# Optimization experiments

Measured on AMD Instinct MI355X. Metric: run time of the kernel, lower is better.

The kernel has to match this reference:

```python
import jax, jax.numpy as jnp
import numpy as np

RADIUS = 51  # odd-ified from 50
WEIGHT = 0.5
THRESHOLD = 10.0


def _gaussian_kernel_2d(k: int) -> np.ndarray:
    # Replicates cv2.getGaussianKernel(k, 0): sigma = 0.3*((k-1)*0.5 - 1) + 0.8
    sigma = 0.3 * ((k - 1) * 0.5 - 1.0) + 0.8
    x = np.arange(k, dtype=np.float64) - (k - 1) / 2.0
    g = np.exp(-(x ** 2) / (2.0 * sigma ** 2))
    g = g / g.sum()
    return np.outer(g, g).astype(np.float32)  # (k, k)


def filter2d(img, kernel):
    # img: (b, c, h, w), kernel: (k, k); depthwise 'same' conv (symmetric zero pad)
    b, c, h, w = img.shape
    k = kernel.shape[-1]
    p = k // 2
    x = img.reshape(b * c, 1, h, w)
    w2 = kernel.reshape(1, 1, k, k).astype(img.dtype)
    out = jax.lax.conv_general_dilated(
        x, w2,
        window_strides=(1, 1),
        padding=[(p, p), (p, p)],
        dimension_numbers=("NCHW", "OIHW", "NCHW"),
    )
    return out.reshape(b, c, h, w)


def setup_inputs() -> dict:
    key = jax.random.key(0)
    img = jax.random.uniform(key, (16, 3, 512, 512), dtype=jnp.float32)
    kernel = jnp.asarray(_gaussian_kernel_2d(RADIUS))
    return {"img": img, "kernel": kernel}


def reference(img, kernel):
    blur = filter2d(img, kernel)
    residual = img - blur
    mask = (jnp.abs(residual) * 255.0 > THRESHOLD).astype(img.dtype)
    soft_mask = filter2d(mask, kernel)
    sharp = jnp.clip(img + WEIGHT * residual, 0.0, 1.0)
    return soft_mask * sharp + (1.0 - soft_mask) * img
```

## Files before the change

kernel.cpp:

```cpp
#include <hip/hip_runtime.h>
#include <hip/hip_fp16.h>
#include <math.h>

#define IMG_H 512
#define IMG_W 512
#define NCH   48
#define KR    51
#define PAD   25
#define WEIGHT 0.5f
#define THRESH 10.0f

struct GK { float g[KR]; };

__device__ __forceinline__ int swz6144(int b) { return (b & 7) * 768 + (b >> 3); }

__device__ __forceinline__ void hblur4(const float* tl, int t, const GK& gk,
                                       float a[4]) {
  a[0] = a[1] = a[2] = a[3] = 0.f;
  #pragma unroll
  for (int m = 0; m < 14; ++m) {
    float4 q = *reinterpret_cast<const float4*>(&tl[4 * t + 4 * m]);
    float qa[4] = {q.x, q.y, q.z, q.w};
    #pragma unroll
    for (int e = 0; e < 4; ++e)
      #pragma unroll
      for (int o = 0; o < 4; ++o) {
        int j = 4 * m + e - o;
        if (j >= 0 && j < KR) a[o] += gk.g[j] * qa[e];
      }
  }
}

template <bool CHK>
__device__ __forceinline__ void vacc4(const __half* p , int y0,
                                      const GK& gk, float acc[4][4]) {
  #pragma unroll
  for (int u = 0; u < 4; ++u)
    acc[u][0] = acc[u][1] = acc[u][2] = acc[u][3] = 0.f;
  #pragma unroll
  for (int d = -PAD; d <= 3 + PAD; ++d) {
    int ry = y0 + d;
    if (CHK && ((unsigned)ry >= (unsigned)IMG_H)) continue;
    union { uint2 u2; __half2 h[2]; } pk;
    pk.u2 = *reinterpret_cast<const uint2*>(p + (size_t)ry * IMG_W);
    float q0 = __low2float(pk.h[0]), q1 = __high2float(pk.h[0]);
    float q2 = __low2float(pk.h[1]), q3 = __high2float(pk.h[1]);
    #pragma unroll
    for (int u = 0; u < 4; ++u) {
      int j = d - u + PAD;
      if (j >= 0 && j < KR) {
        float w = gk.g[j];
        acc[u][0] += w * q0; acc[u][1] += w * q1;
        acc[u][2] += w * q2; acc[u][3] += w * q3;
      }
    }
  }
}

__global__ __launch_bounds__(256, 8) void k1_hblur(const float* __restrict__ in,
                                                   __half* __restrict__ out, GK gk) {
  __shared__ float tile[2][564];
  const int tid = threadIdx.x;
  const int sub = tid >> 7;
  const int t   = tid & 127;
  const int row = blockIdx.x * 2 + sub;
  const float* rin = in + (size_t)row * IMG_W;
  float* tl = tile[sub];
  float4 v = *reinterpret_cast<const float4*>(&rin[4 * t]);
  if (t < 25) tl[t] = 0.f;
  if (t < 27) tl[537 + t] = 0.f;
  tl[25 + 4 * t + 0] = v.x; tl[25 + 4 * t + 1] = v.y;
  tl[25 + 4 * t + 2] = v.z; tl[25 + 4 * t + 3] = v.w;
  __syncthreads();
  float a[4];
  hblur4(tl, t, gk, a);
  union { uint2 u2; __half2 h[2]; } pk;
  pk.h[0] = __floats2half2_rn(a[0], a[1]);
  pk.h[1] = __floats2half2_rn(a[2], a[3]);
  *reinterpret_cast<uint2*>(&out[(size_t)row * IMG_W + 4 * t]) = pk.u2;
}

__global__ __launch_bounds__(128, 5) void k2_vres_hmask(
    const __half* __restrict__ t1, const float* __restrict__ img,
    __half* __restrict__ res, __half* __restrict__ t2, GK gk) {
  const int t  = threadIdx.x;
  const int l  = swz6144(blockIdx.x);
  const int yb = l & 127;
  const int c  = l >> 7;
  const int y0 = yb * 4;
  const int x  = 4 * t;
  const size_t base = (size_t)c * IMG_H * IMG_W;
  float acc[4][4];
  if (y0 >= PAD && y0 + 3 + PAD < IMG_H)
    vacc4<false>(t1 + base + x, y0, gk, acc);
  else
    vacc4<true>(t1 + base + x, y0, gk, acc);

  __shared__ float tl[4][564];
  if (t < 25) { tl[0][t] = 0.f; tl[1][t] = 0.f; tl[2][t] = 0.f; tl[3][t] = 0.f; }
  if (t < 27) {
    tl[0][537 + t] = 0.f; tl[1][537 + t] = 0.f;
    tl[2][537 + t] = 0.f; tl[3][537 + t] = 0.f;
  }
  #pragma unroll
  for (int u = 0; u < 4; ++u) {
    const size_t off = base + (size_t)(y0 + u) * IMG_W + x;
    float4 iv = *reinterpret_cast<const float4*>(&img[off]);
    float r0 = iv.x - acc[u][0], r1 = iv.y - acc[u][1];
    float r2 = iv.z - acc[u][2], r3 = iv.w - acc[u][3];
    union { uint2 u2; __half2 h[2]; } pk;
    pk.h[0] = __floats2half2_rn(r0, r1);
    pk.h[1] = __floats2half2_rn(r2, r3);
    *reinterpret_cast<uint2*>(&res[off]) = pk.u2;
    tl[u][25 + x + 0] = (fabsf(r0) * 255.f > THRESH) ? 1.f : 0.f;
    tl[u][25 + x + 1] = (fabsf(r1) * 255.f > THRESH) ? 1.f : 0.f;
    tl[u][25 + x + 2] = (fabsf(r2) * 255.f > THRESH) ? 1.f : 0.f;
    tl[u][25 + x + 3] = (fabsf(r3) * 255.f > THRESH) ? 1.f : 0.f;
  }
  __syncthreads();
  #pragma unroll
  for (int u = 0; u < 4; ++u) {
    float a[4];
    hblur4(tl[u], t, gk, a);
    union { uint2 u2; __half2 h[2]; } pk;
    pk.h[0] = __floats2half2_rn(a[0], a[1]);
    pk.h[1] = __floats2half2_rn(a[2], a[3]);
    *reinterpret_cast<uint2*>(&t2[base + (size_t)(y0 + u) * IMG_W + x]) = pk.u2;
  }
}

__global__ __launch_bounds__(128, 5) void k3_vfinal(
    const __half* __restrict__ t2, const float* __restrict__ img,
    const __half* __restrict__ res, float* __restrict__ out, GK gk) {
  const int t  = threadIdx.x;
  const int l  = swz6144(blockIdx.x);
  const int yb = l & 127;
  const int c  = l >> 7;
  const int y0 = yb * 4;
  const int x  = 4 * t;
  const size_t base = (size_t)c * IMG_H * IMG_W;
  float acc[4][4];
  if (y0 >= PAD && y0 + 3 + PAD < IMG_H)
    vacc4<false>(t2 + base + x, y0, gk, acc);
  else
    vacc4<true>(t2 + base + x, y0, gk, acc);

  #pragma unroll
  for (int u = 0; u < 4; ++u) {
    const size_t off = base + (size_t)(y0 + u) * IMG_W + x;
    float4 iv = *reinterpret_cast<const float4*>(&img[off]);
    union { uint2 u2; __half2 h[2]; } pk;
    pk.u2 = *reinterpret_cast<const uint2*>(&res[off]);
    float r[4]  = { __low2float(pk.h[0]), __high2float(pk.h[0]),
                    __low2float(pk.h[1]), __high2float(pk.h[1]) };
    float iva[4] = { iv.x, iv.y, iv.z, iv.w };
    float o[4];
    #pragma unroll
    for (int e = 0; e < 4; ++e) {
      float sharp = fminf(fmaxf(iva[e] + WEIGHT * r[e], 0.f), 1.f);
      o[e] = iva[e] + acc[u][e] * (sharp - iva[e]);
    }
    *reinterpret_cast<float4*>(&out[off]) = make_float4(o[0], o[1], o[2], o[3]);
  }
}

extern "C" void kernel_launch(void* const* d_in, const int* in_sizes, int n_in,
                              void* d_out, int out_size, void* d_ws, size_t ws_size,
                              hipStream_t stream) {
  const float* img = (const float*)d_in[0];
  GK gk;
  {
    double sigma = 0.3 * ((KR - 1) * 0.5 - 1.0) + 0.8;
    double gs[KR], sum = 0.0;
    for (int i = 0; i < KR; ++i) {
      double xd = (double)i - (KR - 1) / 2.0;
      gs[i] = exp(-(xd * xd) / (2.0 * sigma * sigma));
      sum += gs[i];
    }
    for (int i = 0; i < KR; ++i) gk.g[i] = (float)(gs[i] / sum);
  }

  const size_t npx = (size_t)NCH * IMG_H * IMG_W;
  __half* tmp1 = (__half*)d_out;
  __half* res  = (__half*)d_ws;
  __half* tmp2 = (__half*)((char*)d_ws + npx * sizeof(__half));

  const int hblocks = NCH * IMG_H / 2;
  const int vblocks = NCH * (IMG_H / 4);

  k1_hblur     <<<hblocks, 256, 0, stream>>>(img, tmp1, gk);
  k2_vres_hmask<<<vblocks, 128, 0, stream>>>(tmp1, img, res, tmp2, gk);
  k3_vfinal    <<<vblocks, 128, 0, stream>>>(tmp2, img, res, (float*)d_out, gk);
}
```

Baseline: 226.4 us.

## Align shared row tiles to 16 bytes, raise occupancy, nontemporal output stores

The left pad of the shared-memory row tile goes from 25 to 28, so each thread's four values start on a 16-byte boundary and can be written with one float4 store instead of four scalar stores. The horizontal blur loop takes one extra float4 step and shifts its tap index to match. The launch-bounds occupancy hint for the two vertical kernels rises from 5 to 6, and the final output uses nontemporal stores. The vertical-kernel fast-path test now uses 28 instead of 25, so a few more blocks take the bounds-checked path; the extra loop step also adds some LDS reads.

```diff
diff --git a/kernel.cpp b/kernel.cpp
--- a/kernel.cpp
+++ b/kernel.cpp
@@ -7,8 +7,12 @@
 #define NCH   48
 #define KR    51
 #define PAD   25
+#define PADL  28
+#define ROWW  568
 #define WEIGHT 0.5f
 #define THRESH 10.0f
+
+typedef float f32x4 __attribute__((ext_vector_type(4)));
 
 struct GK { float g[KR]; };
 
@@ -18,14 +22,14 @@
                                        float a[4]) {
   a[0] = a[1] = a[2] = a[3] = 0.f;
   #pragma unroll
-  for (int m = 0; m < 14; ++m) {
+  for (int m = 0; m < 15; ++m) {
     float4 q = *reinterpret_cast<const float4*>(&tl[4 * t + 4 * m]);
     float qa[4] = {q.x, q.y, q.z, q.w};
     #pragma unroll
     for (int e = 0; e < 4; ++e)
       #pragma unroll
       for (int o = 0; o < 4; ++o) {
-        int j = 4 * m + e - o;
+        int j = 4 * m + e - o - 3;
         if (j >= 0 && j < KR) a[o] += gk.g[j] * qa[e];
       }
   }
@@ -59,7 +63,7 @@
 
 __global__ __launch_bounds__(256, 8) void k1_hblur(const float* __restrict__ in,
                                                    __half* __restrict__ out, GK gk) {
-  __shared__ float tile[2][564];
+  __shared__ float tile[2][ROWW];
   const int tid = threadIdx.x;
   const int sub = tid >> 7;
   const int t   = tid & 127;
@@ -67,10 +71,8 @@
   const float* rin = in + (size_t)row * IMG_W;
   float* tl = tile[sub];
   float4 v = *reinterpret_cast<const float4*>(&rin[4 * t]);
-  if (t < 25) tl[t] = 0.f;
-  if (t < 27) tl[537 + t] = 0.f;
-  tl[25 + 4 * t + 0] = v.x; tl[25 + 4 * t + 1] = v.y;
-  tl[25 + 4 * t + 2] = v.z; tl[25 + 4 * t + 3] = v.w;
+  if (t < 28) { tl[t] = 0.f; tl[PADL + 512 + t] = 0.f; }
+  *reinterpret_cast<float4*>(&tl[PADL + 4 * t]) = v;
   __syncthreads();
   float a[4];
   hblur4(tl, t, gk, a);
@@ -80,7 +82,7 @@
   *reinterpret_cast<uint2*>(&out[(size_t)row * IMG_W + 4 * t]) = pk.u2;
 }
 
-__global__ __launch_bounds__(128, 5) void k2_vres_hmask(
+__global__ __launch_bounds__(128, 6) void k2_vres_hmask(
     const __half* __restrict__ t1, const float* __restrict__ img,
     __half* __restrict__ res, __half* __restrict__ t2, GK gk) {
   const int t  = threadIdx.x;
@@ -91,16 +93,15 @@
   const int x  = 4 * t;
   const size_t base = (size_t)c * IMG_H * IMG_W;
   float acc[4][4];
-  if (y0 >= PAD && y0 + 3 + PAD < IMG_H)
+  if (y0 >= PADL && y0 + 3 + PADL < IMG_H)
     vacc4<false>(t1 + base + x, y0, gk, acc);
   else
     vacc4<true>(t1 + base + x, y0, gk, acc);
 
-  __shared__ float tl[4][564];
-  if (t < 25) { tl[0][t] = 0.f; tl[1][t] = 0.f; tl[2][t] = 0.f; tl[3][t] = 0.f; }
-  if (t < 27) {
-    tl[0][537 + t] = 0.f; tl[1][537 + t] = 0.f;
-    tl[2][537 + t] = 0.f; tl[3][537 + t] = 0.f;
+  __shared__ float tl[4][ROWW];
+  for (int i = t; i < 224; i += 128) {
+    int u = i / 56, k = i % 56;
+    tl[u][k < 28 ? k : 512 + k] = 0.f;
   }
   #pragma unroll
   for (int u = 0; u < 4; ++u) {
@@ -112,10 +113,12 @@
     pk.h[0] = __floats2half2_rn(r0, r1);
     pk.h[1] = __floats2half2_rn(r2, r3);
     *reinterpret_cast<uint2*>(&res[off]) = pk.u2;
-    tl[u][25 + x + 0] = (fabsf(r0) * 255.f > THRESH) ? 1.f : 0.f;
-    tl[u][25 + x + 1] = (fabsf(r1) * 255.f > THRESH) ? 1.f : 0.f;
-    tl[u][25 + x + 2] = (fabsf(r2) * 255.f > THRESH) ? 1.f : 0.f;
-    tl[u][25 + x + 3] = (fabsf(r3) * 255.f > THRESH) ? 1.f : 0.f;
+    float m0 = (fabsf(r0) * 255.f > THRESH) ? 1.f : 0.f;
+    float m1 = (fabsf(r1) * 255.f > THRESH) ? 1.f : 0.f;
+    float m2 = (fabsf(r2) * 255.f > THRESH) ? 1.f : 0.f;
+    float m3 = (fabsf(r3) * 255.f > THRESH) ? 1.f : 0.f;
+    *reinterpret_cast<float4*>(&tl[u][PADL + x]) =
+        make_float4(m0, m1, m2, m3);
   }
   __syncthreads();
   #pragma unroll
@@ -129,7 +132,7 @@
   }
 }
 
-__global__ __launch_bounds__(128, 5) void k3_vfinal(
+__global__ __launch_bounds__(128, 6) void k3_vfinal(
     const __half* __restrict__ t2, const float* __restrict__ img,
     const __half* __restrict__ res, float* __restrict__ out, GK gk) {
   const int t  = threadIdx.x;
@@ -140,7 +143,7 @@
   const int x  = 4 * t;
   const size_t base = (size_t)c * IMG_H * IMG_W;
   float acc[4][4];
-  if (y0 >= PAD && y0 + 3 + PAD < IMG_H)
+  if (y0 >= PADL && y0 + 3 + PADL < IMG_H)
     vacc4<false>(t2 + base + x, y0, gk, acc);
   else
     vacc4<true>(t2 + base + x, y0, gk, acc);
@@ -160,7 +163,8 @@
       float sharp = fminf(fmaxf(iva[e] + WEIGHT * r[e], 0.f), 1.f);
       o[e] = iva[e] + acc[u][e] * (sharp - iva[e]);
     }
-    *reinterpret_cast<float4*>(&out[off]) = make_float4(o[0], o[1], o[2], o[3]);
+    f32x4 ov = { o[0], o[1], o[2], o[3] };
+    __builtin_nontemporal_store(ov, reinterpret_cast<f32x4*>(&out[off]));
   }
 }
 
```

After: 239.2 us. +5.7%, slower.
